# Performance work log

Measured on AMD Instinct MI355X. Metric: run time of the kernel, lower is better.

## Reference

```python
import jax, jax.numpy as jnp
import numpy as np

D = 4096  # input = hidden = output width of the 3-layer MLP


def setup_inputs() -> dict:
    key = jax.random.key(0)
    ks = jax.random.split(key, 7)
    s = 1.0 / np.sqrt(D)
    return {
        "x": jax.random.normal(ks[0], (D,), jnp.float32),
        "W1": jax.random.normal(ks[1], (D, D), jnp.float32) * s,
        "b1": jax.random.normal(ks[2], (D,), jnp.float32) * 0.01,
        "W2": jax.random.normal(ks[3], (D, D), jnp.float32) * s,
        "b2": jax.random.normal(ks[4], (D,), jnp.float32) * 0.01,
        "W3": jax.random.normal(ks[5], (D, D), jnp.float32) * s,
        "b3": jax.random.normal(ks[6], (D,), jnp.float32) * 0.01,
    }


def _lrp_step(R, W, a):
    """Z-rule: R_new = R @ (a[None,:] * W) / z[:,None], with z = W @ a (+ eps*sign).
    Equivalent to the original per-output-neuron Python loop, fully vectorized.
    R: [n_seeds, out_dim], W: [out_dim, in_dim] (torch Linear layout), a: [in_dim]."""
    z = W @ a                              # [out_dim], bias excluded as in original
    z = z + 1e-9 * jnp.sign(z)
    return ((R / z[None, :]) @ W) * a[None, :]   # [n_seeds, in_dim]


def reference(x, W1, b1, W2, b2, W3, b3):
    # Forward pass of the wrapped MLP; hooks store the INPUT to each Linear.
    a0 = x
    a1 = jax.nn.relu(a0 @ W1.T + b1)
    a2 = jax.nn.relu(a1 @ W2.T + b2)
    out = a2 @ W3.T + b3                   # [D]

    # backward_relevance_propagation: one one-hot-scaled seed per output neuron
    # => the stack of seed vectors is diag(out). Propagate all seeds at once.
    R = jnp.diag(out)                      # [D, D]
    for W, a in ((W3, a2), (W2, a1), (W1, a0)):  # layers reversed, matching activations
        R = _lrp_step(R, W, a)
    # R[i] is the input relevance for output neuron i (stacked input_relevance list)
    return out, R
```

## Files before the change

### kernel.cpp

```cpp
#include <hip/hip_runtime.h>
#include <stdint.h>

#define D 4096
#define CAP 2560
#define CTK 80

typedef __attribute__((ext_vector_type(8))) short bf16x8;
typedef __attribute__((ext_vector_type(4))) float f32x4;

#define MFMA16 __builtin_amdgcn_mfma_f32_16x16x32_bf16

__device__ __forceinline__ float sgnf(float z) {
    return (z > 0.f) ? 1.f : ((z < 0.f) ? -1.f : 0.f);
}
__device__ __forceinline__ uint cvtpk(float a, float b) {
    uint r;
    asm("v_cvt_pk_bf16_f32 %0, %1, %2" : "=v"(r) : "v"(a), "v"(b));
    return r;
}
__device__ __forceinline__ void split3_pk(float f0, float f1, uint& hp, uint& mp, uint& lp) {
    hp = cvtpk(f0, f1);
    float h0 = __uint_as_float(hp << 16);
    float h1 = __uint_as_float(hp & 0xffff0000u);
    float r0 = f0 - h0, r1 = f1 - h1;
    mp = cvtpk(r0, r1);
    float m0 = __uint_as_float(mp << 16);
    float m1 = __uint_as_float(mp & 0xffff0000u);
    lp = cvtpk(r0 - m0, r1 - m1);
}

__global__ __launch_bounds__(256) void gemv_blas8(const float* __restrict__ W,
                                                  const float* __restrict__ v,
                                                  const float* __restrict__ bias,
                                                  float* __restrict__ z,
                                                  float* __restrict__ act, int doAct) {
    __shared__ float vs[D];
    {
        const float4* v4 = (const float4*)v;
        float4* s4 = (float4*)vs;
#pragma unroll
        for (int q = 0; q < 4; q++) s4[threadIdx.x + q * 256] = v4[threadIdx.x + q * 256];
    }
    __syncthreads();
    int gid = blockIdx.x * 256 + threadIdx.x;
    int row = gid >> 3;
    int l = gid & 7;
    const float* wr = W + (size_t)row * D + l;
    float wb0[16], wb1[16], wb2[16];
    float acc = 0.f;
#pragma unroll
    for (int u = 0; u < 16; u++) wb0[u] = wr[u * 8];
#pragma unroll
    for (int u = 0; u < 16; u++) wb1[u] = wr[(16 + u) * 8];
#pragma unroll
    for (int c = 0; c < 32; c++) {
        if (c + 2 < 32) {
            float* dst = ((c + 2) % 3 == 0) ? wb0 : ((c + 2) % 3 == 1) ? wb1 : wb2;
#pragma unroll
            for (int u = 0; u < 16; u++) dst[u] = wr[((c + 2) * 16 + u) * 8];
        }
        const float* cur = (c % 3 == 0) ? wb0 : (c % 3 == 1) ? wb1 : wb2;
#pragma unroll
        for (int u = 0; u < 16; u++) acc = fmaf(cur[u], vs[l + (c * 16 + u) * 8], acc);
    }
    float b = acc + __shfl_xor(acc, 4);
    float c2 = b + __shfl_xor(b, 1);
    float s = c2 + __shfl_xor(c2, 2);
    if (l == 0) {
        z[row] = s;
        if (doAct) act[row] = fmaxf(s + bias[row], 0.f);
    }
}

__global__ __launch_bounds__(256) void vecprep32(const float* __restrict__ z1,
                                                 const float* __restrict__ z2,
                                                 const float* __restrict__ z3,
                                                 const float* __restrict__ a1,
                                                 const float* __restrict__ a2,
                                                 const float* __restrict__ b3,
                                                 float* __restrict__ out,
                                                 float* __restrict__ s3,
                                                 float* __restrict__ g2,
                                                 float* __restrict__ g1) {
    int i = blockIdx.x * 256 + threadIdx.x;
    float z3v = z3[i];
    float o = z3v + b3[i];
    out[i] = o;
    s3[i] = o / (z3v + 1e-9f * sgnf(z3v));
    float z2v = z2[i];
    g2[i] = a2[i] / (z2v + 1e-9f * sgnf(z2v));
    float z1v = z1[i];
    g1[i] = a1[i] / (z1v + 1e-9f * sgnf(z1v));
}

__global__ __launch_bounds__(64) void scan2(const float* __restrict__ g2,
                                            const float* __restrict__ g1,
                                            int* __restrict__ idx2, float* __restrict__ g2c,
                                            int* __restrict__ idx1, float* __restrict__ g1c,
                                            int* __restrict__ cnt) {
    int lane = threadIdx.x;
    unsigned long long lt = (lane == 63) ? 0x7fffffffffffffffULL : ((1ULL << lane) - 1ULL);
    int base = 0;
    for (int c = 0; c < 64; ++c) {
        float v = g2[c * 64 + lane];
        bool nz = (v != 0.f);
        unsigned long long mask = __ballot(nz);
        int pre = __popcll(mask & lt);
        if (nz && base + pre < CAP) { idx2[base + pre] = c * 64 + lane; g2c[base + pre] = v; }
        base += __popcll(mask);
    }
    if (base > CAP) base = CAP;
    for (int i = base + lane; i < CAP; i += 64) { idx2[i] = 0; g2c[i] = 0.f; }
    int K2pad = (base + 127) & ~127;
    int b1 = 0;
    for (int c = 0; c < 64; ++c) {
        float v = g1[c * 64 + lane];
        bool nz = (v != 0.f);
        unsigned long long mask = __ballot(nz);
        int pre = __popcll(mask & lt);
        if (nz && b1 + pre < CAP) { idx1[b1 + pre] = c * 64 + lane; g1c[b1 + pre] = v; }
        b1 += __popcll(mask);
    }
    if (b1 > CAP) b1 = CAP;
    for (int i = b1 + lane; i < CAP; i += 64) { idx1[i] = 0; g1c[i] = 0.f; }
    int N1pad = (b1 + 127) & ~127;
    if (lane == 0) {
        cnt[0] = K2pad / 32;
        cnt[1] = N1pad / 32;
        cnt[2] = N1pad;
        cnt[3] = K2pad;
    }
}

__global__ __launch_bounds__(256) void prepA1c(const float* __restrict__ W3,
                                               const float* __restrict__ s3,
                                               const int* __restrict__ idx2,
                                               const float* __restrict__ g2c,
                                               ushort* __restrict__ Ph,
                                               ushort* __restrict__ Pm,
                                               ushort* __restrict__ Pl) {
    size_t ci = (size_t)blockIdx.x * 256 + threadIdx.x;
    int cell = (int)(ci & 1023);
    int kt = (int)((ci >> 10) % CTK);
    int bi2 = (int)(ci / (1024 * CTK));
    int mm = cell >> 6, gg = (cell >> 4) & 3, ri = cell & 15;
    int i = bi2 * 256 + mm * 16 + ri;
    int kc0 = kt * 32 + gg * 8;
    float s = s3[i];
    const float* w3r = W3 + (size_t)i * D;
    float v[8];
#pragma unroll
    for (int j = 0; j < 8; j++) v[j] = w3r[idx2[kc0 + j]] * (s * g2c[kc0 + j]);
    uint hp[4], mp[4], lp[4];
#pragma unroll
    for (int j = 0; j < 4; j++) split3_pk(v[2 * j], v[2 * j + 1], hp[j], mp[j], lp[j]);
    size_t dst = ci * 8;
    uint4 u;
    u.x = hp[0]; u.y = hp[1]; u.z = hp[2]; u.w = hp[3]; *(uint4*)(Ph + dst) = u;
    u.x = mp[0]; u.y = mp[1]; u.z = mp[2]; u.w = mp[3]; *(uint4*)(Pm + dst) = u;
    u.x = lp[0]; u.y = lp[1]; u.z = lp[2]; u.w = lp[3]; *(uint4*)(Pl + dst) = u;
}

__global__ __launch_bounds__(256) void prepB1c(const float* __restrict__ W2,
                                               const int* __restrict__ idx2,
                                               const int* __restrict__ idx1,
                                               ushort* __restrict__ Ph,
                                               ushort* __restrict__ Pm,
                                               ushort* __restrict__ Pl) {
    size_t ci = (size_t)blockIdx.x * 256 + threadIdx.x;
    int cell = (int)(ci & 511);
    int kt = (int)((ci >> 9) % CTK);
    int bi = (int)(ci / (512 * CTK));
    int m = cell >> 6, g = (cell >> 4) & 3, r = cell & 15;
    int col = idx1[bi * 128 + m * 16 + r];
    int kc0 = kt * 32 + g * 8;
    float v[8];
#pragma unroll
    for (int j = 0; j < 8; j++) v[j] = W2[(size_t)idx2[kc0 + j] * D + col];
    uint hp[4], mp[4], lp[4];
#pragma unroll
    for (int j = 0; j < 4; j++) split3_pk(v[2 * j], v[2 * j + 1], hp[j], mp[j], lp[j]);
    size_t dst = ci * 8;
    uint4 u;
    u.x = hp[0]; u.y = hp[1]; u.z = hp[2]; u.w = hp[3]; *(uint4*)(Ph + dst) = u;
    u.x = mp[0]; u.y = mp[1]; u.z = mp[2]; u.w = mp[3]; *(uint4*)(Pm + dst) = u;
    u.x = lp[0]; u.y = lp[1]; u.z = lp[2]; u.w = lp[3]; *(uint4*)(Pl + dst) = u;
}

__global__ __launch_bounds__(256) void prepB2c(const float* __restrict__ W1,
                                               const int* __restrict__ idx1,
                                               ushort* __restrict__ Ph,
                                               ushort* __restrict__ Pm,
                                               ushort* __restrict__ Pl) {
    __shared__ float tile[64][129];
    int bi = blockIdx.x / (CAP / 64);
    int kch = blockIdx.x % (CAP / 64);
    int k0 = kch * 64;
    int c0 = bi * 128;
    int t = threadIdx.x;
#pragma unroll
    for (int q = 0; q < 8; q++) {
        int idx = t + q * 256;
        int rr = idx >> 5;
        int c4 = idx & 31;
        int row = idx1[k0 + rr];
        float4 wv = *(const float4*)(W1 + (size_t)row * D + c0 + c4 * 4);
        tile[rr][c4 * 4 + 0] = wv.x;
        tile[rr][c4 * 4 + 1] = wv.y;
        tile[rr][c4 * 4 + 2] = wv.z;
        tile[rr][c4 * 4 + 3] = wv.w;
    }
    __syncthreads();
#pragma unroll
    for (int q = 0; q < 4; q++) {
        int oi = t + q * 256;
        int ktl = oi >> 9;
        int rem = oi & 511;
        int m = rem >> 6, g = (rem >> 4) & 3, r = rem & 15;
        int col = m * 16 + r;
        float vv[8];
#pragma unroll
        for (int j = 0; j < 8; j++) vv[j] = tile[ktl * 32 + g * 8 + j][col];
        uint hp[4], mp[4], lp[4];
#pragma unroll
        for (int j = 0; j < 4; j++) split3_pk(vv[2 * j], vv[2 * j + 1], hp[j], mp[j], lp[j]);
        size_t dst = (((size_t)bi * CTK + kch * 2 + ktl) * 512 + rem) * 8;
        uint4 u;
        u.x = hp[0]; u.y = hp[1]; u.z = hp[2]; u.w = hp[3]; *(uint4*)(Ph + dst) = u;
        u.x = mp[0]; u.y = mp[1]; u.z = mp[2]; u.w = mp[3]; *(uint4*)(Pm + dst) = u;
        u.x = lp[0]; u.y = lp[1]; u.z = lp[2]; u.w = lp[3]; *(uint4*)(Pl + dst) = u;
    }
}

template <int MODE>
__global__ __launch_bounds__(256, 3) void gemm_c(const ushort* __restrict__ Ah,
                                                 const ushort* __restrict__ Am_,
                                                 const ushort* __restrict__ Al_,
                                                 const ushort* __restrict__ Bh,
                                                 const ushort* __restrict__ Bm_,
                                                 const ushort* __restrict__ Bl_,
                                                 const float* __restrict__ cs,
                                                 const int* __restrict__ cnt,
                                                 float* __restrict__ O,
                                                 ushort* __restrict__ Cph,
                                                 ushort* __restrict__ Cpm,
                                                 ushort* __restrict__ Cpl_) {
    const int NT = cnt[MODE == 1 ? 0 : 1];
    if (MODE == 1 && (int)blockIdx.x * 128 >= cnt[2]) return;
    __shared__ ushort ldsA[3][4096];
    __shared__ ushort ldsB[3][4096];
    int t = threadIdx.x;
    int lane = t & 63, wv = t >> 6;
    int wr = wv >> 1, wc = wv & 1;
    int r = lane & 15, g = lane >> 4;
    int bx = blockIdx.x, by = blockIdx.y;
    size_t row0 = (size_t)by * 128, col0 = (size_t)bx * 128;

    f32x4 acc[4][4];
#pragma unroll
    for (int m = 0; m < 4; m++)
#pragma unroll
        for (int n = 0; n < 4; n++) acc[m][n] = (f32x4){0.f, 0.f, 0.f, 0.f};

    size_t abase = ((size_t)(by >> 1) * CTK) * 8192 + (size_t)(by & 1) * 4096;

    auto DMAA = [&](int kt) {
        size_t at = abase + (size_t)kt * 8192;
        const ushort* asrc[3] = {Ah + at, Am_ + at, Al_ + at};
#pragma unroll
        for (int p = 0; p < 3; p++) {
            __builtin_amdgcn_global_load_lds(
                (const __attribute__((address_space(1))) uint32_t*)(asrc[p] + (size_t)t * 8),
                (__attribute__((address_space(3))) uint32_t*)(&ldsA[p][t * 8]), 16, 0, 0);
            __builtin_amdgcn_global_load_lds(
                (const __attribute__((address_space(1))) uint32_t*)(asrc[p] + (size_t)(t + 256) * 8),
                (__attribute__((address_space(3))) uint32_t*)(&ldsA[p][(t + 256) * 8]), 16, 0, 0);
        }
    };
    auto DMAB = [&](int kt) {
        size_t bt = ((size_t)bx * CTK + kt) * 4096;
        const ushort* bsrc[3] = {Bh + bt, Bm_ + bt, Bl_ + bt};
#pragma unroll
        for (int p = 0; p < 3; p++) {
            __builtin_amdgcn_global_load_lds(
                (const __attribute__((address_space(1))) uint32_t*)(bsrc[p] + (size_t)t * 8),
                (__attribute__((address_space(3))) uint32_t*)(&ldsB[p][t * 8]), 16, 0, 0);
            __builtin_amdgcn_global_load_lds(
                (const __attribute__((address_space(1))) uint32_t*)(bsrc[p] + (size_t)(t + 256) * 8),
                (__attribute__((address_space(3))) uint32_t*)(&ldsB[p][(t + 256) * 8]), 16, 0, 0);
        }
    };

    auto MFMA_PHASE = [&]() {
        __builtin_amdgcn_s_setprio(1);
        bf16x8 bh[4], bm[4], bl[4];
#pragma unroll
        for (int n = 0; n < 4; n++) bh[n] = *(const bf16x8*)&ldsB[0][(wc * 4 + n) * 512 + lane * 8];
#pragma unroll
        for (int n = 0; n < 4; n++) bm[n] = *(const bf16x8*)&ldsB[1][(wc * 4 + n) * 512 + lane * 8];
#pragma unroll
        for (int n = 0; n < 4; n++) bl[n] = *(const bf16x8*)&ldsB[2][(wc * 4 + n) * 512 + lane * 8];
        {
            bf16x8 a[4];
#pragma unroll
            for (int m = 0; m < 4; m++) a[m] = *(const bf16x8*)&ldsA[0][(wr * 4 + m) * 512 + lane * 8];
#pragma unroll
            for (int m = 0; m < 4; m++)
#pragma unroll
                for (int n = 0; n < 4; n++) {
                    acc[m][n] = MFMA16(a[m], bh[n], acc[m][n], 0, 0, 0);
                    acc[m][n] = MFMA16(a[m], bm[n], acc[m][n], 0, 0, 0);
                    acc[m][n] = MFMA16(a[m], bl[n], acc[m][n], 0, 0, 0);
                }
        }
        {
            bf16x8 a[4];
#pragma unroll
            for (int m = 0; m < 4; m++) a[m] = *(const bf16x8*)&ldsA[1][(wr * 4 + m) * 512 + lane * 8];
#pragma unroll
            for (int m = 0; m < 4; m++)
#pragma unroll
                for (int n = 0; n < 4; n++) {
                    acc[m][n] = MFMA16(a[m], bh[n], acc[m][n], 0, 0, 0);
                    acc[m][n] = MFMA16(a[m], bm[n], acc[m][n], 0, 0, 0);
                }
        }
        {
            bf16x8 a[4];
#pragma unroll
            for (int m = 0; m < 4; m++) a[m] = *(const bf16x8*)&ldsA[2][(wr * 4 + m) * 512 + lane * 8];
#pragma unroll
            for (int m = 0; m < 4; m++)
#pragma unroll
                for (int n = 0; n < 4; n++)
                    acc[m][n] = MFMA16(a[m], bh[n], acc[m][n], 0, 0, 0);
        }
        __builtin_amdgcn_s_setprio(0);
    };

    DMAA(0);
    DMAB(0);
    asm volatile("s_waitcnt vmcnt(0)" ::: "memory");
    __builtin_amdgcn_sched_barrier(0);
    __builtin_amdgcn_s_barrier();
    __builtin_amdgcn_sched_barrier(0);

    for (int tt = 0; tt < NT; ++tt) {
        MFMA_PHASE();
        __builtin_amdgcn_sched_barrier(0);
        __builtin_amdgcn_s_barrier();
        __builtin_amdgcn_sched_barrier(0);
        if (tt < NT - 1) {
            DMAA(tt + 1);
            DMAB(tt + 1);
            asm volatile("s_waitcnt vmcnt(0)" ::: "memory");
            __builtin_amdgcn_sched_barrier(0);
            __builtin_amdgcn_s_barrier();
            __builtin_amdgcn_sched_barrier(0);
        }
    }

    float csv[4];
#pragma unroll
    for (int n = 0; n < 4; n++) csv[n] = cs[col0 + wc * 64 + n * 16 + r];
#pragma unroll
    for (int m = 0; m < 4; m++)
#pragma unroll
        for (int n = 0; n < 4; n++) {
            if (MODE == 0) {
#pragma unroll
                for (int j = 0; j < 4; j++) {
                    size_t grow = row0 + wr * 64 + m * 16 + g * 4 + j;
                    size_t gcol = col0 + wc * 64 + n * 16 + r;
                    O[grow * D + gcol] = acc[m][n][j] * csv[n];
                }
            } else {
                float v0 = acc[m][n][0] * csv[n], v1 = acc[m][n][1] * csv[n];
                float v2 = acc[m][n][2] * csv[n], v3 = acc[m][n][3] * csv[n];
                uint hp0, mp0, lp0, hp1, mp1, lp1;
                split3_pk(v0, v1, hp0, mp0, lp0);
                split3_pk(v2, v3, hp1, mp1, lp1);
                int k = (int)(col0 + wc * 64 + n * 16 + r);
                int ktc = k >> 5, gg = (k & 31) >> 3, jj = k & 7;
#pragma unroll
                for (int j = 0; j < 4; j++) {
                    int i = (int)(row0 + wr * 64 + m * 16 + g * 4 + j);
                    int bi = i >> 8, mm = (i & 255) >> 4, ri = i & 15;
                    size_t off = ((size_t)bi * CTK + ktc) * 8192 +
                                 (size_t)(mm * 64 + gg * 16 + ri) * 8 + jj;
                    uint hpk = (j < 2) ? hp0 : hp1;
                    uint mpk = (j < 2) ? mp0 : mp1;
                    uint lpk = (j < 2) ? lp0 : lp1;
                    int sh = (j & 1) * 16;
                    Cph[off] = (ushort)(hpk >> sh);
                    Cpm[off] = (ushort)(mpk >> sh);
                    Cpl_[off] = (ushort)(lpk >> sh);
                }
            }
        }
}

__global__ __launch_bounds__(256) void prepBT(const float* __restrict__ W,
                                              ushort* __restrict__ Ph,
                                              ushort* __restrict__ Pm,
                                              ushort* __restrict__ Pl) {
    __shared__ float tile[64][129];
    int bi = blockIdx.x >> 6;
    int kpair = blockIdx.x & 63;
    int k0 = kpair * 64;
    int c0 = bi * 128;
    int t = threadIdx.x;
#pragma unroll
    for (int q = 0; q < 8; q++) {
        int idx = t + q * 256;
        int rr = idx >> 5;
        int c4 = idx & 31;
        float4 wv = *(const float4*)(W + (size_t)(k0 + rr) * D + c0 + c4 * 4);
        tile[rr][c4 * 4 + 0] = wv.x;
        tile[rr][c4 * 4 + 1] = wv.y;
        tile[rr][c4 * 4 + 2] = wv.z;
        tile[rr][c4 * 4 + 3] = wv.w;
    }
    __syncthreads();
#pragma unroll
    for (int q = 0; q < 4; q++) {
        int oi = t + q * 256;
        int ktl = oi >> 9;
        int rem = oi & 511;
        int m = rem >> 6, g = (rem >> 4) & 3, r = rem & 15;
        int col = m * 16 + r;
        float vv[8];
#pragma unroll
        for (int j = 0; j < 8; j++) vv[j] = tile[ktl * 32 + g * 8 + j][col];
        uint hp[4], mp[4], lp[4];
#pragma unroll
        for (int j = 0; j < 4; j++) split3_pk(vv[2 * j], vv[2 * j + 1], hp[j], mp[j], lp[j]);
        size_t dst = (((size_t)bi * 128 + kpair * 2 + ktl) * 512 + rem) * 8;
        uint4 u;
        u.x = hp[0]; u.y = hp[1]; u.z = hp[2]; u.w = hp[3]; *(uint4*)(Ph + dst) = u;
        u.x = mp[0]; u.y = mp[1]; u.z = mp[2]; u.w = mp[3]; *(uint4*)(Pm + dst) = u;
        u.x = lp[0]; u.y = lp[1]; u.z = lp[2]; u.w = lp[3]; *(uint4*)(Pl + dst) = u;
    }
}

template <int SCALED>
__global__ __launch_bounds__(256, 2) void gemm_bs(const float* __restrict__ A,
                                                  const ushort* __restrict__ Bh,
                                                  const ushort* __restrict__ Bm_,
                                                  const ushort* __restrict__ Bl_,
                                                  const float* __restrict__ rs,
                                                  const float* __restrict__ ks,
                                                  const float* __restrict__ cs,
                                                  float* __restrict__ O) {
    __shared__ ushort ldsA[3][4096];
    __shared__ ushort ldsB[2][3][4096];
    int t = threadIdx.x;
    int lane = t & 63, wv = t >> 6;
    int wr = wv >> 1, wc = wv & 1;
    int r = lane & 15, g = lane >> 4;
    int bx = blockIdx.x, by = blockIdx.y;
    size_t row0 = (size_t)by * 128, col0 = (size_t)bx * 128;
    int rr = t >> 1;
    int kh = t & 1;
    int cellb0 = ((rr >> 4) * 64 + (kh * 2 + 0) * 16 + (rr & 15)) * 8;
    int cellb1 = ((rr >> 4) * 64 + (kh * 2 + 1) * 16 + (rr & 15)) * 8;
    f32x4 acc[4][4];
#pragma unroll
    for (int m = 0; m < 4; m++)
#pragma unroll
        for (int n = 0; n < 4; n++) acc[m][n] = (f32x4){0.f, 0.f, 0.f, 0.f};
    float rsv = SCALED ? rs[row0 + rr] : 0.f;
    const float* arow = A + (row0 + rr) * (size_t)D;
    float av[16];
    auto LOADA = [&](int k0) {
        const float4* pa = (const float4*)(arow + k0 + kh * 16);
#pragma unroll
        for (int qq = 0; qq < 4; qq++) {
            float4 w = pa[qq];
            av[qq * 4 + 0] = w.x; av[qq * 4 + 1] = w.y;
            av[qq * 4 + 2] = w.z; av[qq * 4 + 3] = w.w;
        }
        if (SCALED) {
            const float4* pk = (const float4*)(ks + k0 + kh * 16);
#pragma unroll
            for (int qq = 0; qq < 4; qq++) {
                float4 kk = pk[qq];
                av[qq * 4 + 0] *= rsv * kk.x; av[qq * 4 + 1] *= rsv * kk.y;
                av[qq * 4 + 2] *= rsv * kk.z; av[qq * 4 + 3] *= rsv * kk.w;
            }
        }
    };
    auto DMAB = [&](int kt, int buf) {
        size_t bt = ((size_t)bx * 128 + kt) * 4096;
        const ushort* bsrc[3] = {Bh + bt, Bm_ + bt, Bl_ + bt};
#pragma unroll
        for (int p = 0; p < 3; p++) {
            __builtin_amdgcn_global_load_lds(
                (const __attribute__((address_space(1))) uint32_t*)(bsrc[p] + (size_t)t * 8),
                (__attribute__((address_space(3))) uint32_t*)(&ldsB[buf][p][t * 8]), 16, 0, 0);
            __builtin_amdgcn_global_load_lds(
                (const __attribute__((address_space(1))) uint32_t*)(bsrc[p] + (size_t)(t + 256) * 8),
                (__attribute__((address_space(3))) uint32_t*)(&ldsB[buf][p][(t + 256) * 8]), 16, 0, 0);
        }
    };
    auto SPLITA = [&]() {
        uint hp[8], mp[8], lp[8];
#pragma unroll
        for (int j = 0; j < 8; j++) split3_pk(av[2 * j], av[2 * j + 1], hp[j], mp[j], lp[j]);
        uint4 u;
        u.x = hp[0]; u.y = hp[1]; u.z = hp[2]; u.w = hp[3]; *(uint4*)&ldsA[0][cellb0] = u;
        u.x = hp[4]; u.y = hp[5]; u.z = hp[6]; u.w = hp[7]; *(uint4*)&ldsA[0][cellb1] = u;
        u.x = mp[0]; u.y = mp[1]; u.z = mp[2]; u.w = mp[3]; *(uint4*)&ldsA[1][cellb0] = u;
        u.x = mp[4]; u.y = mp[5]; u.z = mp[6]; u.w = mp[7]; *(uint4*)&ldsA[1][cellb1] = u;
        u.x = lp[0]; u.y = lp[1]; u.z = lp[2]; u.w = lp[3]; *(uint4*)&ldsA[2][cellb0] = u;
        u.x = lp[4]; u.y = lp[5]; u.z = lp[6]; u.w = lp[7]; *(uint4*)&ldsA[2][cellb1] = u;
    };
    auto MFMA_PHASE = [&](int buf) {
        bf16x8 bh[4], bm[4], bl[4];
#pragma unroll
        for (int n = 0; n < 4; n++) bh[n] = *(const bf16x8*)&ldsB[buf][0][(wc * 4 + n) * 512 + lane * 8];
#pragma unroll
        for (int n = 0; n < 4; n++) bm[n] = *(const bf16x8*)&ldsB[buf][1][(wc * 4 + n) * 512 + lane * 8];
#pragma unroll
        for (int n = 0; n < 4; n++) bl[n] = *(const bf16x8*)&ldsB[buf][2][(wc * 4 + n) * 512 + lane * 8];
        {
            bf16x8 a[4];
#pragma unroll
            for (int m = 0; m < 4; m++) a[m] = *(const bf16x8*)&ldsA[0][(wr * 4 + m) * 512 + lane * 8];
#pragma unroll
            for (int m = 0; m < 4; m++)
#pragma unroll
                for (int n = 0; n < 4; n++) {
                    acc[m][n] = MFMA16(a[m], bh[n], acc[m][n], 0, 0, 0);
                    acc[m][n] = MFMA16(a[m], bm[n], acc[m][n], 0, 0, 0);
                    acc[m][n] = MFMA16(a[m], bl[n], acc[m][n], 0, 0, 0);
                }
        }
        {
            bf16x8 a[4];
#pragma unroll
            for (int m = 0; m < 4; m++) a[m] = *(const bf16x8*)&ldsA[1][(wr * 4 + m) * 512 + lane * 8];
#pragma unroll
            for (int m = 0; m < 4; m++)
#pragma unroll
                for (int n = 0; n < 4; n++) {
                    acc[m][n] = MFMA16(a[m], bh[n], acc[m][n], 0, 0, 0);
                    acc[m][n] = MFMA16(a[m], bm[n], acc[m][n], 0, 0, 0);
                }
        }
        {
            bf16x8 a[4];
#pragma unroll
            for (int m = 0; m < 4; m++) a[m] = *(const bf16x8*)&ldsA[2][(wr * 4 + m) * 512 + lane * 8];
#pragma unroll
            for (int m = 0; m < 4; m++)
#pragma unroll
                for (int n = 0; n < 4; n++)
                    acc[m][n] = MFMA16(a[m], bh[n], acc[m][n], 0, 0, 0);
        }
    };
    const int NT = D / 32;
    LOADA(0);
    SPLITA();
    DMAB(0, 0);
    LOADA(32);
    DMAB(1, 1);
    asm volatile("s_waitcnt vmcnt(6) lgkmcnt(0)" ::: "memory");
    __builtin_amdgcn_s_barrier();
    __builtin_amdgcn_sched_barrier(0);
    for (int tt = 0; tt < NT; ++tt) {
        MFMA_PHASE(tt & 1);
        __builtin_amdgcn_sched_barrier(0);
        __builtin_amdgcn_s_barrier();
        __builtin_amdgcn_sched_barrier(0);
        if (tt < NT - 1) {
            SPLITA();
            if (tt < NT - 2) {
                LOADA((tt + 2) * 32);
                DMAB(tt + 2, tt & 1);
                asm volatile("s_waitcnt vmcnt(6) lgkmcnt(0)" ::: "memory");
            } else {
                asm volatile("s_waitcnt vmcnt(0) lgkmcnt(0)" ::: "memory");
            }
            __builtin_amdgcn_s_barrier();
            __builtin_amdgcn_sched_barrier(0);
        }
    }
    float csv[4];
#pragma unroll
    for (int n = 0; n < 4; n++) csv[n] = cs[col0 + wc * 64 + n * 16 + r];
#pragma unroll
    for (int m = 0; m < 4; m++)
#pragma unroll
        for (int n = 0; n < 4; n++)
#pragma unroll
            for (int j = 0; j < 4; j++) {
                size_t grow = row0 + wr * 64 + m * 16 + g * 4 + j;
                size_t gcol = col0 + wc * 64 + n * 16 + r;
                O[grow * D + gcol] = acc[m][n][j] * csv[n];
            }
}

extern "C" void kernel_launch(void* const* d_in, const int* in_sizes, int n_in,
                              void* d_out, int out_size, void* d_ws, size_t ws_size,
                              hipStream_t stream) {
    const float* x = (const float*)d_in[0];
    const float* W1 = (const float*)d_in[1];
    const float* b1 = (const float*)d_in[2];
    const float* W2 = (const float*)d_in[3];
    const float* b2 = (const float*)d_in[4];
    const float* W3 = (const float*)d_in[5];
    const float* b3 = (const float*)d_in[6];

    float* out = (float*)d_out;
    float* Rout = out + D;

    char* ws = (char*)d_ws;
    float* z1 = (float*)ws;
    float* z2 = z1 + D;
    float* z3 = z2 + D;
    float* a1 = z3 + D;
    float* a2 = a1 + D;
    float* s3 = a2 + D;
    float* g2 = s3 + D;
    float* g1 = g2 + D;
    size_t smallB = (size_t)D * 8 * sizeof(float);

    gemv_blas8<<<(D * 8) / 256, 256, 0, stream>>>(W1, x, b1, z1, a1, 1);
    gemv_blas8<<<(D * 8) / 256, 256, 0, stream>>>(W2, a1, b2, z2, a2, 1);
    gemv_blas8<<<(D * 8) / 256, 256, 0, stream>>>(W3, a2, b3, z3, nullptr, 0);
    vecprep32<<<D / 256, 256, 0, stream>>>(z1, z2, z3, a1, a2, b3, out, s3, g2, g1);

    const size_t PLA = (size_t)16 * CTK * 8192;
    const size_t PLB1 = (size_t)20 * CTK * 4096;
    size_t o_scan = smallB;
    size_t o_A1 = o_scan + 65536;
    size_t o_B1 = o_A1 + 3 * PLA * 2;
    size_t o_C = o_B1 + 3 * PLB1 * 2;
    size_t newNeed = o_C + 3 * PLA * 2 + 256;

    const size_t PL = (size_t)D * D;
    size_t need1 = smallB + 3 * PL * 2 + (size_t)D * D * 4 + 256;

    if (ws_size >= newNeed) {
        int* idx2 = (int*)(ws + o_scan);
        float* g2c = (float*)(idx2 + CAP);
        int* idx1 = (int*)(g2c + CAP);
        float* g1c = (float*)(idx1 + CAP);
        int* cnt = (int*)(g1c + CAP);
        ushort* A1 = (ushort*)(ws + o_A1);
        ushort* B1 = (ushort*)(ws + o_B1);
        ushort* Cp = (ushort*)(ws + o_C);
        ushort* B2 = A1;

        scan2<<<1, 64, 0, stream>>>(g2, g1, idx2, g2c, idx1, g1c, cnt);
        prepA1c<<<(int)(16 * CTK * 1024 / 256), 256, 0, stream>>>(W3, s3, idx2, g2c,
                                                                  A1, A1 + PLA, A1 + 2 * PLA);
        prepB1c<<<(int)(20 * CTK * 512 / 256), 256, 0, stream>>>(W2, idx2, idx1,
                                                                 B1, B1 + PLB1, B1 + 2 * PLB1);
        dim3 g1d(CAP / 128, 32);
        gemm_c<1><<<g1d, 256, 0, stream>>>(A1, A1 + PLA, A1 + 2 * PLA,
                                           B1, B1 + PLB1, B1 + 2 * PLB1,
                                           g1c, cnt, nullptr,
                                           Cp, Cp + PLA, Cp + 2 * PLA);
        prepB2c<<<32 * (CAP / 64), 256, 0, stream>>>(W1, idx1, B2, B2 + PLA, B2 + 2 * PLA);
        dim3 g2d(32, 32);
        gemm_c<0><<<g2d, 256, 0, stream>>>(Cp, Cp + PLA, Cp + 2 * PLA,
                                           B2, B2 + PLA, B2 + 2 * PLA,
                                           x, cnt, Rout, nullptr, nullptr, nullptr);
    } else if (ws_size >= need1) {
        ushort* Bpl = (ushort*)(ws + smallB);
        float* C = (float*)(ws + smallB + 3 * PL * 2);
        dim3 gg(D / 128, D / 128);
        int pgrid = (D / 128) * (D / 64);
        prepBT<<<pgrid, 256, 0, stream>>>(W2, Bpl, Bpl + PL, Bpl + 2 * PL);
        gemm_bs<1><<<gg, 256, 0, stream>>>(W3, Bpl, Bpl + PL, Bpl + 2 * PL, s3, g2, g1, C);
        prepBT<<<pgrid, 256, 0, stream>>>(W1, Bpl, Bpl + PL, Bpl + 2 * PL);
        gemm_bs<0><<<gg, 256, 0, stream>>>(C, Bpl, Bpl + PL, Bpl + 2 * PL, nullptr, nullptr, x, Rout);
    }
}
```

Measured before the change: 665.7 us.

## Enlarge compressed GEMM tile to 256x128 with 512-thread blocks and 8 waves

Doubles the M dimension of each block tile from 128 to 256 rows, using 512 threads (8 waves) per block so each staged B tile is reused across twice as many rows. This roughly halves the B-operand global traffic per output and the number of blocks. The MFMA phase is restructured into a helper that multiplies one A-plane against one B-plane, keeping the same six split-precision products. LDS use grows to 72 KB per block and the launch bound asks for 4 blocks per CU, which raises register pressure and may limit occupancy.

Result: slower. 712.4 us (+7.0%).

```diff
diff --git a/kernel.cpp b/kernel.cpp
--- a/kernel.cpp
+++ b/kernel.cpp
@@ -233,28 +233,28 @@
 }
 
 template <int MODE>
-__global__ __launch_bounds__(256, 3) void gemm_c(const ushort* __restrict__ Ah,
-                                                 const ushort* __restrict__ Am_,
-                                                 const ushort* __restrict__ Al_,
-                                                 const ushort* __restrict__ Bh,
-                                                 const ushort* __restrict__ Bm_,
-                                                 const ushort* __restrict__ Bl_,
-                                                 const float* __restrict__ cs,
-                                                 const int* __restrict__ cnt,
-                                                 float* __restrict__ O,
-                                                 ushort* __restrict__ Cph,
-                                                 ushort* __restrict__ Cpm,
-                                                 ushort* __restrict__ Cpl_) {
+__global__ __launch_bounds__(512, 4) void gemm_c2(const ushort* __restrict__ Ah,
+                                                  const ushort* __restrict__ Am_,
+                                                  const ushort* __restrict__ Al_,
+                                                  const ushort* __restrict__ Bh,
+                                                  const ushort* __restrict__ Bm_,
+                                                  const ushort* __restrict__ Bl_,
+                                                  const float* __restrict__ cs,
+                                                  const int* __restrict__ cnt,
+                                                  float* __restrict__ O,
+                                                  ushort* __restrict__ Cph,
+                                                  ushort* __restrict__ Cpm,
+                                                  ushort* __restrict__ Cpl_) {
     const int NT = cnt[MODE == 1 ? 0 : 1];
     if (MODE == 1 && (int)blockIdx.x * 128 >= cnt[2]) return;
-    __shared__ ushort ldsA[3][4096];
+    __shared__ ushort ldsA[3][8192];
     __shared__ ushort ldsB[3][4096];
     int t = threadIdx.x;
     int lane = t & 63, wv = t >> 6;
-    int wr = wv >> 1, wc = wv & 1;
+    int wm = wv >> 1, wn = wv & 1;
     int r = lane & 15, g = lane >> 4;
     int bx = blockIdx.x, by = blockIdx.y;
-    size_t row0 = (size_t)by * 128, col0 = (size_t)bx * 128;
+    size_t row0 = (size_t)by * 256, col0 = (size_t)bx * 128;
 
     f32x4 acc[4][4];
 #pragma unroll
@@ -262,7 +262,7 @@
 #pragma unroll
         for (int n = 0; n < 4; n++) acc[m][n] = (f32x4){0.f, 0.f, 0.f, 0.f};
 
-    size_t abase = ((size_t)(by >> 1) * CTK) * 8192 + (size_t)(by & 1) * 4096;
+    size_t abase = (size_t)by * CTK * 8192;
 
     auto DMAA = [&](int kt) {
         size_t at = abase + (size_t)kt * 8192;
@@ -273,8 +273,8 @@
                 (const __attribute__((address_space(1))) uint32_t*)(asrc[p] + (size_t)t * 8),
                 (__attribute__((address_space(3))) uint32_t*)(&ldsA[p][t * 8]), 16, 0, 0);
             __builtin_amdgcn_global_load_lds(
-                (const __attribute__((address_space(1))) uint32_t*)(asrc[p] + (size_t)(t + 256) * 8),
-                (__attribute__((address_space(3))) uint32_t*)(&ldsA[p][(t + 256) * 8]), 16, 0, 0);
+                (const __attribute__((address_space(1))) uint32_t*)(asrc[p] + (size_t)(t + 512) * 8),
+                (__attribute__((address_space(3))) uint32_t*)(&ldsA[p][(t + 512) * 8]), 16, 0, 0);
         }
     };
     auto DMAB = [&](int kt) {
@@ -285,56 +285,32 @@
             __builtin_amdgcn_global_load_lds(
                 (const __attribute__((address_space(1))) uint32_t*)(bsrc[p] + (size_t)t * 8),
                 (__attribute__((address_space(3))) uint32_t*)(&ldsB[p][t * 8]), 16, 0, 0);
-            __builtin_amdgcn_global_load_lds(
-                (const __attribute__((address_space(1))) uint32_t*)(bsrc[p] + (size_t)(t + 256) * 8),
-                (__attribute__((address_space(3))) uint32_t*)(&ldsB[p][(t + 256) * 8]), 16, 0, 0);
-        }
+        }
+    };
+
+    auto PROD = [&](int pa, int pb) {
+        bf16x8 a[4], b[4];
+#pragma unroll
+        for (int n = 0; n < 4; n++)
+            b[n] = *(const bf16x8*)&ldsB[pb][((wn * 4 + n) * 64 + lane) * 8];
+#pragma unroll
+        for (int m = 0; m < 4; m++)
+            a[m] = *(const bf16x8*)&ldsA[pa][((wm * 4 + m) * 64 + lane) * 8];
+#pragma unroll
+        for (int m = 0; m < 4; m++)
+#pragma unroll
+            for (int n = 0; n < 4; n++)
+                acc[m][n] = MFMA16(a[m], b[n], acc[m][n], 0, 0, 0);
     };
 
     auto MFMA_PHASE = [&]() {
         __builtin_amdgcn_s_setprio(1);
-        bf16x8 bh[4], bm[4], bl[4];
-#pragma unroll
-        for (int n = 0; n < 4; n++) bh[n] = *(const bf16x8*)&ldsB[0][(wc * 4 + n) * 512 + lane * 8];
-#pragma unroll
-        for (int n = 0; n < 4; n++) bm[n] = *(const bf16x8*)&ldsB[1][(wc * 4 + n) * 512 + lane * 8];
-#pragma unroll
-        for (int n = 0; n < 4; n++) bl[n] = *(const bf16x8*)&ldsB[2][(wc * 4 + n) * 512 + lane * 8];
-        {
-            bf16x8 a[4];
-#pragma unroll
-            for (int m = 0; m < 4; m++) a[m] = *(const bf16x8*)&ldsA[0][(wr * 4 + m) * 512 + lane * 8];
-#pragma unroll
-            for (int m = 0; m < 4; m++)
-#pragma unroll
-                for (int n = 0; n < 4; n++) {
-                    acc[m][n] = MFMA16(a[m], bh[n], acc[m][n], 0, 0, 0);
-                    acc[m][n] = MFMA16(a[m], bm[n], acc[m][n], 0, 0, 0);
-                    acc[m][n] = MFMA16(a[m], bl[n], acc[m][n], 0, 0, 0);
-                }
-        }
-        {
-            bf16x8 a[4];
-#pragma unroll
-            for (int m = 0; m < 4; m++) a[m] = *(const bf16x8*)&ldsA[1][(wr * 4 + m) * 512 + lane * 8];
-#pragma unroll
-            for (int m = 0; m < 4; m++)
-#pragma unroll
-                for (int n = 0; n < 4; n++) {
-                    acc[m][n] = MFMA16(a[m], bh[n], acc[m][n], 0, 0, 0);
-                    acc[m][n] = MFMA16(a[m], bm[n], acc[m][n], 0, 0, 0);
-                }
-        }
-        {
-            bf16x8 a[4];
-#pragma unroll
-            for (int m = 0; m < 4; m++) a[m] = *(const bf16x8*)&ldsA[2][(wr * 4 + m) * 512 + lane * 8];
-#pragma unroll
-            for (int m = 0; m < 4; m++)
-#pragma unroll
-                for (int n = 0; n < 4; n++)
-                    acc[m][n] = MFMA16(a[m], bh[n], acc[m][n], 0, 0, 0);
-        }
+        PROD(0, 0);
+        PROD(0, 1);
+        PROD(1, 0);
+        PROD(1, 1);
+        PROD(0, 2);
+        PROD(2, 0);
         __builtin_amdgcn_s_setprio(0);
     };
 
@@ -362,7 +338,7 @@
 
     float csv[4];
 #pragma unroll
-    for (int n = 0; n < 4; n++) csv[n] = cs[col0 + wc * 64 + n * 16 + r];
+    for (int n = 0; n < 4; n++) csv[n] = cs[col0 + wn * 64 + n * 16 + r];
 #pragma unroll
     for (int m = 0; m < 4; m++)
 #pragma unroll
@@ -370,8 +346,8 @@
             if (MODE == 0) {
 #pragma unroll
                 for (int j = 0; j < 4; j++) {
-                    size_t grow = row0 + wr * 64 + m * 16 + g * 4 + j;
-                    size_t gcol = col0 + wc * 64 + n * 16 + r;
+                    size_t grow = row0 + wm * 64 + m * 16 + g * 4 + j;
+                    size_t gcol = col0 + wn * 64 + n * 16 + r;
                     O[grow * D + gcol] = acc[m][n][j] * csv[n];
                 }
             } else {
@@ -380,11 +356,11 @@
                 uint hp0, mp0, lp0, hp1, mp1, lp1;
                 split3_pk(v0, v1, hp0, mp0, lp0);
                 split3_pk(v2, v3, hp1, mp1, lp1);
-                int k = (int)(col0 + wc * 64 + n * 16 + r);
+                int k = (int)(col0 + wn * 64 + n * 16 + r);
                 int ktc = k >> 5, gg = (k & 31) >> 3, jj = k & 7;
 #pragma unroll
                 for (int j = 0; j < 4; j++) {
-                    int i = (int)(row0 + wr * 64 + m * 16 + g * 4 + j);
+                    int i = (int)(row0 + wm * 64 + m * 16 + g * 4 + j);
                     int bi = i >> 8, mm = (i & 255) >> 4, ri = i & 15;
                     size_t off = ((size_t)bi * CTK + ktc) * 8192 +
                                  (size_t)(mm * 64 + gg * 16 + ri) * 8 + jj;
@@ -658,16 +634,16 @@
                                                                   A1, A1 + PLA, A1 + 2 * PLA);
         prepB1c<<<(int)(20 * CTK * 512 / 256), 256, 0, stream>>>(W2, idx2, idx1,
                                                                  B1, B1 + PLB1, B1 + 2 * PLB1);
-        dim3 g1d(CAP / 128, 32);
-        gemm_c<1><<<g1d, 256, 0, stream>>>(A1, A1 + PLA, A1 + 2 * PLA,
-                                           B1, B1 + PLB1, B1 + 2 * PLB1,
-                                           g1c, cnt, nullptr,
-                                           Cp, Cp + PLA, Cp + 2 * PLA);
+        dim3 g1d(CAP / 128, 16);
+        gemm_c2<1><<<g1d, 512, 0, stream>>>(A1, A1 + PLA, A1 + 2 * PLA,
+                                            B1, B1 + PLB1, B1 + 2 * PLB1,
+                                            g1c, cnt, nullptr,
+                                            Cp, Cp + PLA, Cp + 2 * PLA);
         prepB2c<<<32 * (CAP / 64), 256, 0, stream>>>(W1, idx1, B2, B2 + PLA, B2 + 2 * PLA);
-        dim3 g2d(32, 32);
-        gemm_c<0><<<g2d, 256, 0, stream>>>(Cp, Cp + PLA, Cp + 2 * PLA,
-                                           B2, B2 + PLA, B2 + 2 * PLA,
-                                           x, cnt, Rout, nullptr, nullptr, nullptr);
+        dim3 g2d(32, 16);
+        gemm_c2<0><<<g2d, 512, 0, stream>>>(Cp, Cp + PLA, Cp + 2 * PLA,
+                                            B2, B2 + PLA, B2 + 2 * PLA,
+                                            x, cnt, Rout, nullptr, nullptr, nullptr);
     } else if (ws_size >= need1) {
         ushort* Bpl = (ushort*)(ws + smallB);
         float* C = (float*)(ws + smallB + 3 * PL * 2);
```
